# Performance work log

Measured on AMD Instinct MI355X. Metric: run time of the kernel, lower is better.

The kernel has to match this reference:

```python
import jax, jax.numpy as jnp
import numpy as np
from jax import lax

GAIN = 2.0 ** (-0.5)
EPS = 1e-8


def _modconv(x, style_vec, s_w, s_b, weight):
    # x: [b, cin, h, w]; style_vec: [b, style_dim]
    # s_w: [cin, style_dim], s_b: [cin]; weight: [cout, cin, k, k]
    style_dim = s_w.shape[1]
    scale = GAIN * style_dim ** (-0.5)  # EqualizedLinear scale on input
    style = (style_vec * scale) @ s_w.T + s_b            # [b, cin]
    w = weight[None] * style[:, None, :, None, None]     # [b, cout, cin, k, k]
    demod = lax.rsqrt(jnp.sum(w * w, axis=(2, 3, 4)) + EPS)  # [b, cout]
    w = w * demod[:, :, None, None, None]

    def conv_one(xi, wi):
        # xi: [cin, h, w], wi: [cout, cin, k, k]
        return lax.conv_general_dilated(
            xi[None], wi, window_strides=(1, 1), padding='SAME',
            dimension_numbers=('NCHW', 'OIHW', 'NCHW'))[0]

    return jax.vmap(conv_one)(x, w)  # [b, cout, h, w]


def setup_inputs() -> dict:
    key = jax.random.key(0)
    ks = jax.random.split(key, 13)
    B, Cin, Cout, S, H, W = 16, 256, 256, 512, 64, 64
    f32 = jnp.float32
    return {
        'x': jax.random.normal(ks[0], (B, Cin, H, W), f32),
        'w1': jax.random.normal(ks[1], (B, S), f32),
        'w2': jax.random.normal(ks[2], (B, S), f32),
        'noise1': jax.random.normal(ks[3], (B, 1, H, W), f32),
        'noise2': jax.random.normal(ks[4], (B, 1, H, W), f32),
        's1_w': jax.random.normal(ks[5], (Cin, S), f32),
        's1_b': jnp.zeros((Cin,), f32),
        'conv1_w': jax.random.normal(ks[6], (Cout, Cin, 3, 3), f32),
        'nw1': 0.1 * jax.random.normal(ks[7], (Cout,), f32),
        's2_w': jax.random.normal(ks[8], (Cout, S), f32),
        's2_b': jnp.zeros((Cout,), f32),
        'conv2_w': jax.random.normal(ks[9], (Cout, Cout, 3, 3), f32),
        'nw2': 0.1 * jax.random.normal(ks[10], (Cout,), f32),
    }


def reference(x, w1, w2, noise1, noise2, s1_w, s1_b, conv1_w, nw1,
              s2_w, s2_b, conv2_w, nw2):
    h = _modconv(x, w1, s1_w, s1_b, conv1_w)
    h = h + nw1[None, :, None, None] * noise1
    h = jax.nn.leaky_relu(h, 0.2)
    h = _modconv(h, w2, s2_w, s2_b, conv2_w)
    h = h + nw2[None, :, None, None] * noise2
    return jax.nn.leaky_relu(h, 0.2)
```

## Files before the change

### kernel.cpp

```cpp
#include <hip/hip_runtime.h>
#include <cstdint>
#include <cstddef>

typedef _Float16 f16;
typedef _Float16 f16x8 __attribute__((ext_vector_type(8)));
typedef _Float16 f16x4 __attribute__((ext_vector_type(4)));
typedef float    f32x4 __attribute__((ext_vector_type(4)));

typedef const void __attribute__((address_space(1))) gconst_void;
typedef void __attribute__((address_space(3)))       lds_void;

#define LDS_IN_HALF_ELEMS (6*66*40)
#define LDS_IN_BYTES      (2*6*66*40*2)
#define WBUF_BYTES        32768
#define SMEM_TOTAL        (LDS_IN_BYTES + 2*WBUF_BYTES)
#define WF_BYTES          37748736ULL

__device__ __forceinline__ int lin_idx(int half, int row, int col, int ci) {
    return ((half*6 + row)*66 + col)*40 + ci;
}

__device__ __forceinline__ void gll16(const char* g, char* l) {
    __builtin_amdgcn_global_load_lds((gconst_void*)g, (lds_void*)l, 16, 0, 0);
}

__global__ __launch_bounds__(256) void prep_kernel(
    const float* __restrict__ style_vec,
    const float* __restrict__ s_w,
    const float* __restrict__ s_b,
    const float* __restrict__ conv_w,
    f16* __restrict__ wf)
{
    const int b = blockIdx.x & 15;
    const int g = blockIdx.x >> 4;
    const int t = threadIdx.x;
    __shared__ float style[256];
    {
        const float4* sv = (const float4*)(style_vec + b*512);
        const float4* sw = (const float4*)(s_w + (size_t)t*512);
        float acc = 0.f;
        for (int i = 0; i < 128; ++i) {
            float4 a = sv[i], w = sw[i];
            acc += a.x*w.x + a.y*w.y + a.z*w.z + a.w*w.w;
        }
        style[t] = acc * 0.03125f + s_b[t];
    }
    __syncthreads();

    const int cout = g*32 + (t >> 3);
    const int sub  = t & 7;
    const int cin0 = sub * 32;
    const float* wrow = conv_w + (size_t)cout * 2304;

    float ss = 0.f;
    for (int ci = 0; ci < 32; ++ci) {
        float st = style[cin0 + ci];
        const float* wp = wrow + (cin0 + ci)*9;
        #pragma unroll
        for (int kk = 0; kk < 9; ++kk) { float v = wp[kk]*st; ss += v*v; }
    }
    ss += __shfl_xor(ss, 1);
    ss += __shfl_xor(ss, 2);
    ss += __shfl_xor(ss, 4);
    const float dem = 64.f / sqrtf(ss + 1e-8f);

    const int cg = cout >> 4;
    const int lane_lo = cout & 15;
    for (int kg = 0; kg < 4; ++kg) {
        float stv[8];
        #pragma unroll
        for (int j = 0; j < 8; ++j) stv[j] = style[cin0 + kg*8 + j] * dem;
        for (int kk = 0; kk < 9; ++kk) {
            f16x8 hi, lo;
            #pragma unroll
            for (int j = 0; j < 8; ++j) {
                float v = wrow[(cin0 + kg*8 + j)*9 + kk] * stv[j];
                f16 h = (f16)v;
                hi[j] = h;
                lo[j] = (f16)(v - (float)h);
            }
            size_t base = ((((size_t)(b*9 + kk)*8 + sub)*16 + cg)*2)*512
                        + (size_t)(lane_lo + 16*kg)*8;
            *(f16x8*)(wf + base)       = hi;
            *(f16x8*)(wf + base + 512) = lo;
        }
    }
}

template<int MODE>
__global__ __launch_bounds__(512, 2) void conv_kernel(
    const float*    __restrict__ in32,
    const uint32_t* __restrict__ in_pair,
    const f16*      __restrict__ wf,
    const float*    __restrict__ noise,
    const float*    __restrict__ nw,
    float*          __restrict__ out32,
    uint32_t*       __restrict__ out_pair)
{
    extern __shared__ __align__(16) char smem[];
    f16*  lds_in = (f16*)smem;
    char* wbuf   = smem + LDS_IN_BYTES;

    const int tid  = threadIdx.x;
    const int b    = blockIdx.x & 15;
    const int y0   = (blockIdx.x >> 4) * 4;
    const int lane = tid & 63;
    const int wave = tid >> 6;
    const int wm   = wave & 1;
    const int wn   = wave >> 1;
    const int lcol = lane & 15;
    const int kg   = lane >> 4;

    for (int e = tid; e < 2*6*2*40; e += 512) {
        int half = e / 480; int rem = e - half*480;
        int row = rem / 80; int rem2 = rem - row*80;
        int side = rem2 / 40; int ci = rem2 - side*40;
        lds_in[lin_idx(half, row, side ? 65 : 0, ci)] = (f16)0.f;
    }

    f32x4 acc[8][4];
    #pragma unroll
    for (int m = 0; m < 8; ++m)
        #pragma unroll
        for (int n = 0; n < 4; ++n)
            acc[m][n] = (f32x4){0.f, 0.f, 0.f, 0.f};

    const int y = y0 + wn;
    float nz[4];
    #pragma unroll
    for (int n = 0; n < 4; ++n) nz[n] = noise[b*4096 + y*64 + n*16 + lcol];

    const char* wf_b = (const char*)wf + (size_t)b * 9 * 8 * WBUF_BYTES;

    #pragma unroll 1
    for (int ck = 0; ck < 8; ++ck) {
        __syncthreads();

        #pragma unroll
        for (int i = 0; i < 6; ++i) {
            int grp = i*512 + tid;
            int col, row, ci0;
            if (MODE == 0) { col = grp & 63; row = (grp >> 6) % 6; ci0 = (grp / 384) * 4; }
            else           { ci0 = (grp & 7) * 4; col = (grp >> 3) & 63; row = grp >> 9; }
            int gy = y0 - 1 + row;
            f16x4 hi4 = (f16x4){(f16)0.f,(f16)0.f,(f16)0.f,(f16)0.f};
            f16x4 lo4 = hi4;
            if (gy >= 0 && gy < 64) {
                if (MODE == 0) {
                    const float* p = in32 + ((size_t)(b*256 + ck*32 + ci0))*4096 + gy*64 + col;
                    #pragma unroll
                    for (int k = 0; k < 4; ++k) {
                        float xv = p[(size_t)k*4096] * 64.f;
                        f16 h = (f16)xv;
                        hi4[k] = h;
                        lo4[k] = (f16)(xv - (float)h);
                    }
                } else {
                    const f16x8 pr = *(const f16x8*)(in_pair +
                        ((size_t)((b*8 + ck)*64 + gy)*64 + col)*32 + ci0);
                    hi4 = __builtin_shufflevector(pr, pr, 0, 2, 4, 6);
                    lo4 = __builtin_shufflevector(pr, pr, 1, 3, 5, 7);
                }
            }
            *(f16x4*)(lds_in + lin_idx(0, row, col + 1, ci0)) = hi4;
            *(f16x4*)(lds_in + lin_idx(1, row, col + 1, ci0)) = lo4;
        }

        {
            const char* gsw = wf_b + (size_t)(0*8 + ck) * WBUF_BYTES;
            char* lsw = wbuf;
            #pragma unroll
            for (int r = 0; r < 4; ++r) {
                int off = (r*512 + tid) * 16;
                gll16(gsw + off, lsw + off);
            }
        }

        #pragma unroll 1
        for (int t = 0; t < 9; ++t) {
            __syncthreads();
            if (t < 8) {
                const char* gsw = wf_b + (size_t)((t+1)*8 + ck) * WBUF_BYTES;
                char* lsw = wbuf + ((t+1)&1) * WBUF_BYTES;
                #pragma unroll
                for (int r = 0; r < 4; ++r) {
                    int off = (r*512 + tid) * 16;
                    gll16(gsw + off, lsw + off);
                }
            }
            const int kh = t / 3, kw = t - kh*3;
            const f16* wcur = (const f16*)(wbuf + (t&1) * WBUF_BYTES);

            f16x8 bhi[4], blo[4];
            #pragma unroll
            for (int n = 0; n < 4; ++n) {
                int e = ((wn + kh)*66 + n*16 + lcol + kw)*40 + kg*8;
                bhi[n] = *(const f16x8*)(lds_in + e);
                blo[n] = *(const f16x8*)(lds_in + e + LDS_IN_HALF_ELEMS);
            }
            #pragma unroll
            for (int m = 0; m < 8; ++m) {
                const f16* ap = wcur + (size_t)((wm*8 + m)*2)*512 + lane*8;
                f16x8 ahi = *(const f16x8*)ap;
                f16x8 alo = *(const f16x8*)(ap + 512);
                #pragma unroll
                for (int n = 0; n < 4; ++n) {
                    acc[m][n] = __builtin_amdgcn_mfma_f32_16x16x32_f16(ahi, bhi[n], acc[m][n], 0, 0, 0);
                    acc[m][n] = __builtin_amdgcn_mfma_f32_16x16x32_f16(ahi, blo[n], acc[m][n], 0, 0, 0);
                    acc[m][n] = __builtin_amdgcn_mfma_f32_16x16x32_f16(alo, bhi[n], acc[m][n], 0, 0, 0);
                }
            }
        }
    }

    const float inv = 1.f / 4096.f;
    #pragma unroll
    for (int m = 0; m < 8; ++m) {
        const int coutb = wm*128 + m*16 + kg*4;
        float nwv[4];
        #pragma unroll
        for (int r = 0; r < 4; ++r) nwv[r] = nw[coutb + r];
        #pragma unroll
        for (int n = 0; n < 4; ++n) {
            const int col = n*16 + lcol;
            #pragma unroll
            for (int r = 0; r < 4; ++r) {
                float v = acc[m][n][r]*inv + nwv[r]*nz[n];
                v = fmaxf(v, 0.2f*v);
                const int cout = coutb + r;
                if (MODE == 0) {
                    float vs = v * 64.f;
                    f16 h = (f16)vs;
                    f16 l = (f16)(vs - (float)h);
                    uint32_t pk = (uint32_t)__builtin_bit_cast(uint16_t, h)
                                | ((uint32_t)__builtin_bit_cast(uint16_t, l) << 16);
                    size_t idx = (((size_t)(b*8 + (cout >> 5))*64 + y)*64 + col)*32 + (cout & 31);
                    out_pair[idx] = pk;
                } else {
                    out32[((size_t)(b*256 + cout))*4096 + y*64 + col] = v;
                }
            }
        }
    }
}

extern "C" void kernel_launch(void* const* d_in, const int* in_sizes, int n_in,
                              void* d_out, int out_size, void* d_ws, size_t ws_size,
                              hipStream_t stream) {
    (void)in_sizes; (void)n_in; (void)out_size; (void)ws_size;
    const float* x      = (const float*)d_in[0];
    const float* w1     = (const float*)d_in[1];
    const float* w2     = (const float*)d_in[2];
    const float* noise1 = (const float*)d_in[3];
    const float* noise2 = (const float*)d_in[4];
    const float* s1w    = (const float*)d_in[5];
    const float* s1b    = (const float*)d_in[6];
    const float* c1w    = (const float*)d_in[7];
    const float* nw1    = (const float*)d_in[8];
    const float* s2w    = (const float*)d_in[9];
    const float* s2b    = (const float*)d_in[10];
    const float* c2w    = (const float*)d_in[11];
    const float* nw2    = (const float*)d_in[12];
    float* out = (float*)d_out;

    f16*      wf    = (f16*)d_ws;
    uint32_t* hpair = (uint32_t*)((char*)d_ws + WF_BYTES);

    (void)hipFuncSetAttribute(reinterpret_cast<const void*>(&conv_kernel<0>),
                              hipFuncAttributeMaxDynamicSharedMemorySize, SMEM_TOTAL);
    (void)hipFuncSetAttribute(reinterpret_cast<const void*>(&conv_kernel<1>),
                              hipFuncAttributeMaxDynamicSharedMemorySize, SMEM_TOTAL);

    prep_kernel<<<128, 256, 0, stream>>>(w1, s1w, s1b, c1w, wf);
    conv_kernel<0><<<256, 512, SMEM_TOTAL, stream>>>(x, nullptr, wf, noise1, nw1, nullptr, hpair);
    prep_kernel<<<128, 256, 0, stream>>>(w2, s2w, s2b, c2w, wf);
    conv_kernel<1><<<256, 512, SMEM_TOTAL, stream>>>(nullptr, hpair, wf, noise2, nw2, out, nullptr);
}
```

Baseline: 617.6 us.

## Drop weight lo-split, split output channels across blocks, pipeline weight tiles

```diff
diff --git a/kernel.cpp b/kernel.cpp
--- a/kernel.cpp
+++ b/kernel.cpp
@@ -12,9 +12,9 @@
 
 #define LDS_IN_HALF_ELEMS (6*66*40)
 #define LDS_IN_BYTES      (2*6*66*40*2)
-#define WBUF_BYTES        32768
-#define SMEM_TOTAL        (LDS_IN_BYTES + 2*WBUF_BYTES)
-#define WF_BYTES          37748736ULL
+#define WTILE_BYTES       8192
+#define SMEM_TOTAL        (LDS_IN_BYTES + 2*WTILE_BYTES)
+#define WF_BYTES          (16ULL*144*8192)
 
 __device__ __forceinline__ int lin_idx(int half, int row, int col, int ci) {
     return ((half*6 + row)*66 + col)*40 + ci;
@@ -64,31 +64,29 @@
     ss += __shfl_xor(ss, 4);
     const float dem = 64.f / sqrtf(ss + 1e-8f);
 
-    const int cg = cout >> 4;
+    const int ch = cout >> 7;
+    const int m  = (cout >> 4) & 7;
     const int lane_lo = cout & 15;
+    const size_t bch_base = ((size_t)b*144 + ch) * 4096;
+
     for (int kg = 0; kg < 4; ++kg) {
         float stv[8];
         #pragma unroll
         for (int j = 0; j < 8; ++j) stv[j] = style[cin0 + kg*8 + j] * dem;
         for (int kk = 0; kk < 9; ++kk) {
-            f16x8 hi, lo;
-            #pragma unroll
-            for (int j = 0; j < 8; ++j) {
-                float v = wrow[(cin0 + kg*8 + j)*9 + kk] * stv[j];
-                f16 h = (f16)v;
-                hi[j] = h;
-                lo[j] = (f16)(v - (float)h);
-            }
-            size_t base = ((((size_t)(b*9 + kk)*8 + sub)*16 + cg)*2)*512
-                        + (size_t)(lane_lo + 16*kg)*8;
-            *(f16x8*)(wf + base)       = hi;
-            *(f16x8*)(wf + base + 512) = lo;
+            f16x8 hi;
+            #pragma unroll
+            for (int j = 0; j < 8; ++j)
+                hi[j] = (f16)(wrow[(cin0 + kg*8 + j)*9 + kk] * stv[j]);
+            size_t off = bch_base + (size_t)((kk*8 + sub)*2) * 4096
+                       + (size_t)(m*64 + lane_lo + 16*kg) * 8;
+            *(f16x8*)(wf + off) = hi;
         }
     }
 }
 
 template<int MODE>
-__global__ __launch_bounds__(512, 2) void conv_kernel(
+__global__ __launch_bounds__(256, 2) void conv_kernel(
     const float*    __restrict__ in32,
     const uint32_t* __restrict__ in_pair,
     const f16*      __restrict__ wf,
@@ -102,16 +100,27 @@
     char* wbuf   = smem + LDS_IN_BYTES;
 
     const int tid  = threadIdx.x;
-    const int b    = blockIdx.x & 15;
-    const int y0   = (blockIdx.x >> 4) * 4;
+    const int bid  = blockIdx.x;
+    const int b    = bid & 15;
+    const int y0   = ((bid >> 4) & 15) * 4;
+    const int ch   = bid >> 8;
     const int lane = tid & 63;
-    const int wave = tid >> 6;
-    const int wm   = wave & 1;
-    const int wn   = wave >> 1;
+    const int wn   = tid >> 6;
     const int lcol = lane & 15;
     const int kg   = lane >> 4;
 
-    for (int e = tid; e < 2*6*2*40; e += 512) {
+    const char* wf_bch = (const char*)wf + ((size_t)b*144 + ch) * WTILE_BYTES;
+
+    auto stage_w = [&](int ck_, int t_, int buf_) {
+        const char* gsw = wf_bch + (size_t)((t_*8 + ck_)*2) * WTILE_BYTES;
+        char* lsw = wbuf + buf_ * WTILE_BYTES;
+        gll16(gsw + tid*16, lsw + tid*16);
+        gll16(gsw + 4096 + tid*16, lsw + 4096 + tid*16);
+    };
+
+    stage_w(0, 0, 0);
+
+    for (int e = tid; e < 2*6*2*40; e += 256) {
         int half = e / 480; int rem = e - half*480;
         int row = rem / 80; int rem2 = rem - row*80;
         int side = rem2 / 40; int ci = rem2 - side*40;
@@ -130,15 +139,13 @@
     #pragma unroll
     for (int n = 0; n < 4; ++n) nz[n] = noise[b*4096 + y*64 + n*16 + lcol];
 
-    const char* wf_b = (const char*)wf + (size_t)b * 9 * 8 * WBUF_BYTES;
-
     #pragma unroll 1
     for (int ck = 0; ck < 8; ++ck) {
         __syncthreads();
 
-        #pragma unroll
-        for (int i = 0; i < 6; ++i) {
-            int grp = i*512 + tid;
+        #pragma unroll 3
+        for (int i = 0; i < 12; ++i) {
+            int grp = i*256 + tid;
             int col, row, ci0;
             if (MODE == 0) { col = grp & 63; row = (grp >> 6) % 6; ci0 = (grp / 384) * 4; }
             else           { ci0 = (grp & 7) * 4; col = (grp >> 3) & 63; row = grp >> 9; }
@@ -166,30 +173,16 @@
             *(f16x4*)(lds_in + lin_idx(1, row, col + 1, ci0)) = lo4;
         }
 
-        {
-            const char* gsw = wf_b + (size_t)(0*8 + ck) * WBUF_BYTES;
-            char* lsw = wbuf;
-            #pragma unroll
-            for (int r = 0; r < 4; ++r) {
-                int off = (r*512 + tid) * 16;
-                gll16(gsw + off, lsw + off);
-            }
-        }
-
-        #pragma unroll 1
+        __syncthreads();
+
+        #pragma unroll
         for (int t = 0; t < 9; ++t) {
-            __syncthreads();
-            if (t < 8) {
-                const char* gsw = wf_b + (size_t)((t+1)*8 + ck) * WBUF_BYTES;
-                char* lsw = wbuf + ((t+1)&1) * WBUF_BYTES;
-                #pragma unroll
-                for (int r = 0; r < 4; ++r) {
-                    int off = (r*512 + tid) * 16;
-                    gll16(gsw + off, lsw + off);
-                }
-            }
+            if (t) __syncthreads();
+            if (t < 8)        stage_w(ck, t+1, (ck + t + 1) & 1);
+            else if (ck < 7)  stage_w(ck+1, 0, (ck + 1) & 1);
+
             const int kh = t / 3, kw = t - kh*3;
-            const f16* wcur = (const f16*)(wbuf + (t&1) * WBUF_BYTES);
+            const f16* wcur = (const f16*)(wbuf + ((ck + t) & 1) * WTILE_BYTES);
 
             f16x8 bhi[4], blo[4];
             #pragma unroll
@@ -198,25 +191,24 @@
                 bhi[n] = *(const f16x8*)(lds_in + e);
                 blo[n] = *(const f16x8*)(lds_in + e + LDS_IN_HALF_ELEMS);
             }
+            __builtin_amdgcn_s_setprio(1);
             #pragma unroll
             for (int m = 0; m < 8; ++m) {
-                const f16* ap = wcur + (size_t)((wm*8 + m)*2)*512 + lane*8;
-                f16x8 ahi = *(const f16x8*)ap;
-                f16x8 alo = *(const f16x8*)(ap + 512);
+                f16x8 a = *(const f16x8*)(wcur + m*512 + lane*8);
                 #pragma unroll
                 for (int n = 0; n < 4; ++n) {
-                    acc[m][n] = __builtin_amdgcn_mfma_f32_16x16x32_f16(ahi, bhi[n], acc[m][n], 0, 0, 0);
-                    acc[m][n] = __builtin_amdgcn_mfma_f32_16x16x32_f16(ahi, blo[n], acc[m][n], 0, 0, 0);
-                    acc[m][n] = __builtin_amdgcn_mfma_f32_16x16x32_f16(alo, bhi[n], acc[m][n], 0, 0, 0);
+                    acc[m][n] = __builtin_amdgcn_mfma_f32_16x16x32_f16(a, bhi[n], acc[m][n], 0, 0, 0);
+                    acc[m][n] = __builtin_amdgcn_mfma_f32_16x16x32_f16(a, blo[n], acc[m][n], 0, 0, 0);
                 }
             }
+            __builtin_amdgcn_s_setprio(0);
         }
     }
 
     const float inv = 1.f / 4096.f;
     #pragma unroll
     for (int m = 0; m < 8; ++m) {
-        const int coutb = wm*128 + m*16 + kg*4;
+        const int coutb = ch*128 + m*16 + kg*4;
         float nwv[4];
         #pragma unroll
         for (int r = 0; r < 4; ++r) nwv[r] = nw[coutb + r];
@@ -272,7 +264,7 @@
                               hipFuncAttributeMaxDynamicSharedMemorySize, SMEM_TOTAL);
 
     prep_kernel<<<128, 256, 0, stream>>>(w1, s1w, s1b, c1w, wf);
-    conv_kernel<0><<<256, 512, SMEM_TOTAL, stream>>>(x, nullptr, wf, noise1, nw1, nullptr, hpair);
+    conv_kernel<0><<<512, 256, SMEM_TOTAL, stream>>>(x, nullptr, wf, noise1, nw1, nullptr, hpair);
     prep_kernel<<<128, 256, 0, stream>>>(w2, s2w, s2b, c2w, wf);
-    conv_kernel<1><<<256, 512, SMEM_TOTAL, stream>>>(nullptr, hpair, wf, noise2, nw2, out, nullptr);
-}
+    conv_kernel<1><<<512, 256, SMEM_TOTAL, stream>>>(nullptr, hpair, wf, noise2, nw2, out, nullptr);
+}
```

Measured after the change: 535.1 us. 1.15x faster.
